# Optimization experiments

Hardware: AMD Instinct MI355X
Metric: run time of the kernel (lower is better)

## Reference

```python
import jax, jax.numpy as jnp
import numpy as np

B, S, DIM = 2, 2048, 2048
NH, NKV = 16, 8
HD = DIM // NH  # 128
ROPE_THETA = 10000.0


def setup_inputs() -> dict:
    key = jax.random.key(0)
    ks = jax.random.split(key, 7)
    std = DIM ** -0.5
    x = jax.random.normal(ks[0], (B, S, DIM), jnp.float32)
    wq = jax.random.normal(ks[1], (NH * HD, DIM), jnp.float32) * std
    wk = jax.random.normal(ks[2], (NKV * HD, DIM), jnp.float32) * std
    wv = jax.random.normal(ks[3], (NKV * HD, DIM), jnp.float32) * std
    wo = jax.random.normal(ks[4], (DIM, NH * HD), jnp.float32) * std
    inv_freq = 1.0 / (ROPE_THETA ** (jnp.arange(0, HD, 2, dtype=jnp.float32) / HD))
    ang = jnp.arange(S, dtype=jnp.float32)[:, None] * inv_freq[None, :]  # [S, HD//2]
    freqs_cos = jnp.cos(ang)
    freqs_sin = jnp.sin(ang)
    # diffusion-style random per-batch token mask: t ~ U[0,1) per batch row
    t = jax.random.uniform(ks[5], (B, 1))
    mask = jax.random.uniform(ks[6], (B, S)) < t  # True = masked key
    mask = mask.at[:, 0].set(False)  # first token never masked
    return dict(x=x, wq=wq, wk=wk, wv=wv, wo=wo,
                freqs_cos=freqs_cos, freqs_sin=freqs_sin, mask=mask)


def _rope(x, cos, sin):
    # x: [b, s, h, d]; pairs (x[2i], x[2i+1]) rotated by angle[s, i]
    xr, xi = x[..., 0::2], x[..., 1::2]
    c = cos[None, :, None, :]
    s = sin[None, :, None, :]
    out = jnp.stack([xr * c - xi * s, xr * s + xi * c], axis=-1)
    return out.reshape(x.shape)


def reference(x, wq, wk, wv, wo, freqs_cos, freqs_sin, mask):
    b, s, _ = x.shape
    xq = jnp.einsum('bsd,ed->bse', x, wq).reshape(b, s, NH, HD)
    xk = jnp.einsum('bsd,ed->bse', x, wk).reshape(b, s, NKV, HD)
    xv = jnp.einsum('bsd,ed->bse', x, wv).reshape(b, s, NKV, HD)
    xq = _rope(xq, freqs_cos, freqs_sin)
    xk = _rope(xk, freqs_cos, freqs_sin)
    n_rep = NH // NKV
    xk = jnp.repeat(xk, n_rep, axis=2)  # repeat_kv (GQA)
    xv = jnp.repeat(xv, n_rep, axis=2)
    q = xq.transpose(0, 2, 1, 3)  # [b, h, s, d]
    k = xk.transpose(0, 2, 1, 3)
    v = xv.transpose(0, 2, 1, 3)
    scale = 1.0 / np.sqrt(HD).astype(np.float32)
    scores = jnp.einsum('bhqd,bhkd->bhqk', q, k) * scale  # [b, h, s, s]
    scores = jnp.where(mask[:, None, None, :], -jnp.inf, scores)
    probs = jax.nn.softmax(scores, axis=-1)
    out = jnp.einsum('bhqk,bhkd->bhqd', probs, v)
    out = out.transpose(0, 2, 1, 3).reshape(b, s, NH * HD)
    return jnp.einsum('bse,de->bsd', out, wo)
```

## Files before the change

### kernel.cpp

```cpp
#include <hip/hip_runtime.h>
#include <hip/hip_bf16.h>
#include <cstdint>
#include <cstddef>

#define S_LEN   2048
#define NHQ     16
#define NKV_H   8
#define HD_DIM  128
#define DMODEL  2048
#define BATCH   2
#define KVD     (NKV_H * HD_DIM)
#define QKV_LD  4096

typedef float f32x4  __attribute__((ext_vector_type(4)));
typedef __bf16 bf16x8 __attribute__((ext_vector_type(8)));
typedef __bf16 bf16x4 __attribute__((ext_vector_type(4)));

__device__ __forceinline__ void gload_lds16(const __bf16* g, __bf16* l) {
    __builtin_amdgcn_global_load_lds(
        (const __attribute__((address_space(1))) void*)g,
        (__attribute__((address_space(3))) void*)l, 16, 0, 0);
}

__global__ void sniff_x_kernel(const unsigned* __restrict__ x,
                               int* __restrict__ flag) {
    __shared__ int cnt;
    if (threadIdx.x == 0) cnt = 0;
    __syncthreads();
    int c = 0;
    for (int j = threadIdx.x; j < 1024; j += 256) {
        unsigned hw = x[j] & 0xFFFFu;
        unsigned e  = (hw >> 7) & 0xFF;
        if (hw == 0u || (e >= 118 && e <= 132)) c++;
    }
    atomicAdd(&cnt, c);
    __syncthreads();
    if (threadIdx.x == 0) *flag = (cnt > 512) ? 1 : 0;
}

__global__ void sniff_fc_kernel(const unsigned* __restrict__ fc,
                                int* __restrict__ flag) {
    if (threadIdx.x == 0) *flag = (fc[0] == 0x3F803F80u) ? 1 : 0;
}

__global__ void mask_norm_kernel(const unsigned char* __restrict__ mraw,
                                 unsigned char* __restrict__ mout, int n) {
    __shared__ int f_bf16, f_f32, f_u8;
    if (threadIdx.x == 0) { f_bf16 = 0; f_f32 = 0; f_u8 = 0; }
    __syncthreads();
    const unsigned* dw = (const unsigned*)mraw;
    int ndw = n / 4;
    for (int j = threadIdx.x; j < ndw; j += blockDim.x) {
        unsigned v = dw[j];
        if (v == 0x00003F80u || v == 0x3F803F80u) f_bf16 = 1;
        else if (v == 0x3F800000u) f_f32 = 1;
        else if (v & 0xFFFFFFFEu) f_u8 = 1;
    }
    __syncthreads();
    int layout;
    if (f_bf16) layout = 3;
    else if (f_f32) layout = 2;
    else if (f_u8) layout = 0;
    else layout = 1;
    for (int i = threadIdx.x; i < n; i += blockDim.x) {
        unsigned v;
        if (layout == 0)      v = mraw[i];
        else if (layout == 3) v = ((const unsigned short*)mraw)[i];
        else                  v = ((const unsigned*)mraw)[i];
        mout[i] = v ? 1u : 0u;
    }
}

__global__ __launch_bounds__(256)
void conv_bf16_kernel(const void* __restrict__ src, __bf16* __restrict__ dst,
                      int n8, const int* __restrict__ dflag) {
    int i = blockIdx.x * blockDim.x + threadIdx.x;
    if (i >= n8) return;
    size_t off = (size_t)i * 8;
    if (*dflag) {
        *reinterpret_cast<uint4*>(dst + off) =
            *reinterpret_cast<const uint4*>((const __bf16*)src + off);
    } else {
        const float* f = (const float*)src + off;
        float4 a = *reinterpret_cast<const float4*>(f);
        float4 b = *reinterpret_cast<const float4*>(f + 4);
        bf16x8 v;
        v[0] = (__bf16)a.x; v[1] = (__bf16)a.y; v[2] = (__bf16)a.z; v[3] = (__bf16)a.w;
        v[4] = (__bf16)b.x; v[5] = (__bf16)b.y; v[6] = (__bf16)b.z; v[7] = (__bf16)b.w;
        *reinterpret_cast<bf16x8*>(dst + off) = v;
    }
}

__global__ __launch_bounds__(256)
void conv_bf16_strided_kernel(const void* __restrict__ src,
                              __bf16* __restrict__ dstbase,
                              int n8, const int* __restrict__ dflag) {
    int i = blockIdx.x * blockDim.x + threadIdx.x;
    if (i >= n8) return;
    size_t off = (size_t)i * 8;
    size_t row = off >> 11;
    size_t col = off & 2047;
    __bf16* dst = dstbase + row * QKV_LD + col;
    if (*dflag) {
        *reinterpret_cast<uint4*>(dst) =
            *reinterpret_cast<const uint4*>((const __bf16*)src + off);
    } else {
        const float* f = (const float*)src + off;
        float4 a = *reinterpret_cast<const float4*>(f);
        float4 b = *reinterpret_cast<const float4*>(f + 4);
        bf16x8 v;
        v[0] = (__bf16)a.x; v[1] = (__bf16)a.y; v[2] = (__bf16)a.z; v[3] = (__bf16)a.w;
        v[4] = (__bf16)b.x; v[5] = (__bf16)b.y; v[6] = (__bf16)b.z; v[7] = (__bf16)b.w;
        *reinterpret_cast<bf16x8*>(dst) = v;
    }
}

template <bool OUT_BF16>
__global__ __launch_bounds__(256)
void gemm_bt_async(const __bf16* __restrict__ A, const __bf16* __restrict__ Bw,
                   void* __restrict__ Cv, int K, int lda, int ldb, int ldc) {
    __shared__ __align__(16) __bf16 As[128 * 64];
    __shared__ __align__(16) __bf16 Bs[128 * 64];

    const int t    = threadIdx.x;
    const int w    = t >> 6;
    const int lane = t & 63;
    const int quad = lane >> 4;
    const int l16  = lane & 15;
    const int wm   = (w >> 1) * 64;
    const int wn   = (w & 1) * 64;
    const int m0   = blockIdx.x * 128;
    const int n0   = blockIdx.y * 128;
    const int rl   = lane >> 3;
    const int gl   = lane & 7;

    f32x4 acc[4][4];
#pragma unroll
    for (int i = 0; i < 4; ++i)
#pragma unroll
        for (int j = 0; j < 4; ++j) acc[i][j] = (f32x4){0.f, 0.f, 0.f, 0.f};

    for (int k0 = 0; k0 < K; k0 += 64) {
        __syncthreads();
#pragma unroll
        for (int p = 0; p < 4; ++p) {
            const int rowb = w * 32 + p * 8;
            const int r    = rowb + rl;
            const int gA   = gl ^ rl;
            gload_lds16(A  + (size_t)(m0 + r) * lda + k0 + gA * 8, &As[rowb * 64]);
            gload_lds16(Bw + (size_t)(n0 + r) * ldb + k0 + gA * 8, &Bs[rowb * 64]);
        }
        __syncthreads();
#pragma unroll
        for (int ks = 0; ks < 2; ++ks) {
            const int G = ks * 4 + quad;
            const int gsw = (G ^ (l16 & 7)) * 8;
            bf16x8 af[4], bf[4];
#pragma unroll
            for (int i = 0; i < 4; ++i)
                af[i] = *reinterpret_cast<const bf16x8*>(
                    &As[(wm + i * 16 + l16) * 64 + gsw]);
#pragma unroll
            for (int j = 0; j < 4; ++j)
                bf[j] = *reinterpret_cast<const bf16x8*>(
                    &Bs[(wn + j * 16 + l16) * 64 + gsw]);
#pragma unroll
            for (int i = 0; i < 4; ++i)
#pragma unroll
                for (int j = 0; j < 4; ++j)
                    acc[i][j] = __builtin_amdgcn_mfma_f32_16x16x32_bf16(
                        af[i], bf[j], acc[i][j], 0, 0, 0);
        }
    }
#pragma unroll
    for (int i = 0; i < 4; ++i)
#pragma unroll
        for (int r = 0; r < 4; ++r) {
            size_t m = (size_t)(m0 + wm + i * 16 + quad * 4 + r);
#pragma unroll
            for (int j = 0; j < 4; ++j) {
                int n = n0 + wn + j * 16 + l16;
                if constexpr (OUT_BF16)
                    ((__hip_bfloat16*)Cv)[m * ldc + n] = __float2bfloat16(acc[i][j][r]);
                else
                    ((float*)Cv)[m * ldc + n] = acc[i][j][r];
            }
        }
}

__global__ void rope_kernel(__hip_bfloat16* __restrict__ xqk,
                            const void* __restrict__ cosv,
                            const void* __restrict__ sinv,
                            const int* __restrict__ dflag_fc,
                            int npairs) {
    int idx = blockIdx.x * blockDim.x + threadIdx.x;
    if (idx >= npairs) return;
    int i  = idx & 63;
    int h  = (idx >> 6) % 24;
    int bs = idx / (64 * 24);
    int s  = bs & (S_LEN - 1);
    float c, sn;
    if (*dflag_fc) {
        c  = __bfloat162float(((const __hip_bfloat16*)cosv)[s * 64 + i]);
        sn = __bfloat162float(((const __hip_bfloat16*)sinv)[s * 64 + i]);
    } else {
        c  = ((const float*)cosv)[s * 64 + i];
        sn = ((const float*)sinv)[s * 64 + i];
    }
    unsigned* p = (unsigned*)(xqk + (size_t)bs * QKV_LD + h * HD_DIM) + i;
    unsigned u = *p;
    float xr = __uint_as_float(u << 16);
    float xi = __uint_as_float(u & 0xFFFF0000u);
    float o0 = xr * c - xi * sn;
    float o1 = xr * sn + xi * c;
    union { __hip_bfloat16 h2[2]; unsigned u32; } out;
    out.h2[0] = __float2bfloat16(o0);
    out.h2[1] = __float2bfloat16(o1);
    *p = out.u32;
}

__global__ __launch_bounds__(256)
void transpose_v_kernel(const __hip_bfloat16* __restrict__ xv,
                        __hip_bfloat16* __restrict__ vt) {
    __shared__ unsigned short T[32][36];
    const int t  = threadIdx.x;
    const int s0 = blockIdx.x * 32;
    const int d0 = blockIdx.y * 32;
    const int z  = blockIdx.z;
    const int b  = z >> 3;
    const int kv = z & 7;
    {
        int sr = t >> 3, dc = (t & 7) * 4;
        const unsigned short* p = (const unsigned short*)xv
            + (size_t)(b * S_LEN + s0 + sr) * QKV_LD + kv * 128 + d0 + dc;
        uint2 v = *reinterpret_cast<const uint2*>(p);
        T[sr][dc + 0] = (unsigned short)(v.x & 0xFFFFu);
        T[sr][dc + 1] = (unsigned short)(v.x >> 16);
        T[sr][dc + 2] = (unsigned short)(v.y & 0xFFFFu);
        T[sr][dc + 3] = (unsigned short)(v.y >> 16);
    }
    __syncthreads();
    {
        int dr = t >> 3, sc = (t & 7) * 4;
        unsigned w0 = (unsigned)T[sc + 0][dr] | ((unsigned)T[sc + 1][dr] << 16);
        unsigned w1 = (unsigned)T[sc + 2][dr] | ((unsigned)T[sc + 3][dr] << 16);
        unsigned short* q = (unsigned short*)vt
            + ((size_t)z * 128 + d0 + dr) * S_LEN + s0 + sc;
        uint2 v; v.x = w0; v.y = w1;
        *reinterpret_cast<uint2*>(q) = v;
    }
}

__global__ __launch_bounds__(256)
void attn_mfma2_kernel(__hip_bfloat16* qkv,
                       const __hip_bfloat16* __restrict__ vt_g,
                       const unsigned char* __restrict__ msk) {
    __shared__ __align__(16) __bf16 Ks[64 * 128];
    __shared__ __align__(16) __bf16 Vt[128 * 64];
    __shared__ __align__(16) __bf16 Ps[4][16][64];

    const int t    = threadIdx.x;
    const int w    = t >> 6;
    const int lane = t & 63;
    const int quad = lane >> 4;
    const int l16  = lane & 15;

    const int bid = blockIdx.x;
    const int qt  = bid & 31;
    const int h   = (bid >> 5) & (NHQ - 1);
    const int b   = bid >> 9;
    const int kvh = h >> 1;
    const int q0  = qt * 64;

    bf16x8 qf[4];
    {
        const __bf16* qrow = (const __bf16*)qkv
            + (size_t)(b * S_LEN + q0 + w * 16 + l16) * QKV_LD + h * 128 + quad * 8;
#pragma unroll
        for (int ks = 0; ks < 4; ++ks)
            qf[ks] = *reinterpret_cast<const bf16x8*>(qrow + ks * 32);
    }

    float m_r = -INFINITY, l_r = 0.f;
    f32x4 o[8];
#pragma unroll
    for (int d0 = 0; d0 < 8; ++d0) o[d0] = (f32x4){0.f, 0.f, 0.f, 0.f};

    const float scale2 = 0.08838834764831845f * 1.4426950408889634f;

    const __bf16* xk = (const __bf16*)qkv + 2048;

    const int krl = lane >> 4, kgl = lane & 15;
    const int vrl = lane >> 3, vgl = lane & 7;
    const int gbase = lane & 48;

    for (int k0 = 0; k0 < S_LEN; k0 += 64) {
        __syncthreads();
#pragma unroll
        for (int p = 0; p < 4; ++p) {
            const int row  = w * 16 + p * 4 + krl;
            const int srcg = kgl ^ (row & 7);
            gload_lds16(xk + (size_t)(b * S_LEN + k0 + row) * QKV_LD
                            + kvh * 128 + srcg * 8,
                        &Ks[(w * 16 + p * 4) * 128]);
        }
#pragma unroll
        for (int p = 0; p < 4; ++p) {
            const int row  = w * 32 + p * 8 + vrl;
            const int srcg = vgl ^ (row & 7);
            gload_lds16((const __bf16*)vt_g
                            + ((size_t)(b * NKV_H + kvh) * 128 + row) * S_LEN
                            + k0 + srcg * 8,
                        &Vt[(w * 32 + p * 8) * 64]);
        }
        unsigned mk4[4];
        {
            const unsigned* mp = (const unsigned*)(msk + b * S_LEN + k0);
#pragma unroll
            for (int n0 = 0; n0 < 4; ++n0) mk4[n0] = mp[n0 * 4 + quad];
        }
        __syncthreads();

        f32x4 sc4[4];
#pragma unroll
        for (int n0 = 0; n0 < 4; ++n0) sc4[n0] = (f32x4){0.f, 0.f, 0.f, 0.f};
        __builtin_amdgcn_s_setprio(1);
#pragma unroll
        for (int ks = 0; ks < 4; ++ks) {
            const int G = ks * 4 + quad;
#pragma unroll
            for (int n0 = 0; n0 < 4; ++n0) {
                const int row  = n0 * 16 + l16;
                const int slot = G ^ (row & 7);
                bf16x8 kf = *reinterpret_cast<const bf16x8*>(&Ks[row * 128 + slot * 8]);
                sc4[n0] = __builtin_amdgcn_mfma_f32_16x16x32_bf16(kf, qf[ks], sc4[n0], 0, 0, 0);
            }
        }
        __builtin_amdgcn_s_setprio(0);

#pragma unroll
        for (int n0 = 0; n0 < 4; ++n0)
#pragma unroll
            for (int r = 0; r < 4; ++r)
                sc4[n0][r] = ((mk4[n0] >> (r * 8)) & 0xFF) ? -INFINITY : sc4[n0][r];

        float tq[4];
#pragma unroll
        for (int n0 = 0; n0 < 4; ++n0)
            tq[n0] = fmaxf(fmaxf(sc4[n0][0], sc4[n0][1]),
                           fmaxf(sc4[n0][2], sc4[n0][3]));
        float rm = fmaxf(fmaxf(tq[0], tq[1]), fmaxf(tq[2], tq[3]));
        rm = fmaxf(rm, __shfl_xor(rm, 16, 64));
        rm = fmaxf(rm, __shfl_xor(rm, 32, 64));

        bool need = (rm - m_r) * scale2 > 8.0f;
        if (__any((int)need)) {
            float mn = fmaxf(m_r, rm);
            float al = exp2f((m_r - mn) * scale2);
            m_r = mn;
            l_r *= al;
            float alq[4];
#pragma unroll
            for (int r = 0; r < 4; ++r)
                alq[r] = __shfl(al, gbase | (quad * 4 + r), 64);
#pragma unroll
            for (int d0 = 0; d0 < 8; ++d0)
#pragma unroll
                for (int r = 0; r < 4; ++r) o[d0][r] *= alq[r];
        }

        float negm = -m_r * scale2;
#pragma unroll
        for (int n0 = 0; n0 < 4; ++n0)
#pragma unroll
            for (int r = 0; r < 4; ++r) {
                float p = exp2f(fmaf(sc4[n0][r], scale2, negm));
                sc4[n0][r] = p;
                l_r += p;
            }

#pragma unroll
        for (int n0 = 0; n0 < 4; ++n0) {
            const int kb    = n0 * 16 + quad * 4;
            const int gran  = kb >> 3;
            const int half4 = kb & 4;
            const int slot  = gran ^ (l16 & 7);
            bf16x4 pk;
            pk[0] = (__bf16)sc4[n0][0];
            pk[1] = (__bf16)sc4[n0][1];
            pk[2] = (__bf16)sc4[n0][2];
            pk[3] = (__bf16)sc4[n0][3];
            *reinterpret_cast<bf16x4*>(&Ps[w][l16][slot * 8 + half4]) = pk;
        }

        __builtin_amdgcn_s_setprio(1);
#pragma unroll
        for (int kk = 0; kk < 64; kk += 32) {
            const int Gp    = (kk >> 3) + quad;
            const int slotp = Gp ^ (l16 & 7);
            bf16x8 af = *reinterpret_cast<const bf16x8*>(&Ps[w][l16][slotp * 8]);
#pragma unroll
            for (int d0 = 0; d0 < 8; ++d0) {
                const int row  = d0 * 16 + l16;
                const int slot = Gp ^ (row & 7);
                bf16x8 bf = *reinterpret_cast<const bf16x8*>(&Vt[row * 64 + slot * 8]);
                o[d0] = __builtin_amdgcn_mfma_f32_16x16x32_bf16(af, bf, o[d0], 0, 0, 0);
            }
        }
        __builtin_amdgcn_s_setprio(0);
    }

    float ls = l_r;
    ls += __shfl_xor(ls, 16, 64);
    ls += __shfl_xor(ls, 32, 64);
    float invl = 1.f / ls;
    float invq[4];
#pragma unroll
    for (int r = 0; r < 4; ++r)
        invq[r] = __shfl(invl, gbase | (quad * 4 + r), 64);
    __hip_bfloat16* att = qkv;
#pragma unroll
    for (int d0 = 0; d0 < 8; ++d0)
#pragma unroll
        for (int r = 0; r < 4; ++r) {
            size_t row = (size_t)(b * S_LEN + q0 + w * 16 + quad * 4 + r);
            att[row * QKV_LD + h * 128 + d0 * 16 + l16] =
                __float2bfloat16(o[d0][r] * invq[r]);
        }
}

extern "C" void kernel_launch(void* const* d_in, const int* in_sizes, int n_in,
                              void* d_out, int out_size, void* d_ws, size_t ws_size,
                              hipStream_t stream) {
    const void* x  = d_in[0];
    const void* wq = d_in[1];
    const void* wk = d_in[2];
    const void* wv = d_in[3];
    const void* wo = d_in[4];
    const void* fc = d_in[5];
    const void* fs = d_in[6];
    const unsigned char* mraw = (const unsigned char*)d_in[7];

    const int M = BATCH * S_LEN;
    char* wsb = (char*)d_ws;
    int* dflag_x  = (int*)wsb;
    int* dflag_fc = (int*)(wsb + 64);
    unsigned char* mnorm = (unsigned char*)(wsb + 128);
    __hip_bfloat16* qkv = (__hip_bfloat16*)(wsb + 8192);

    char* dob = (char*)d_out;
    __bf16* xb    = (__bf16*)dob;
    __bf16* wcomb = (__bf16*)(dob + (16u << 20));
    __bf16* wqb = wcomb;
    __bf16* wkb = wcomb + (size_t)2048 * 2048;
    __bf16* wvb = wcomb + (size_t)3072 * 2048;
    __hip_bfloat16* vt = (__hip_bfloat16*)d_out;

    hipLaunchKernelGGL(sniff_x_kernel, dim3(1), dim3(256), 0, stream,
                       (const unsigned*)x, dflag_x);
    hipLaunchKernelGGL(sniff_fc_kernel, dim3(1), dim3(64), 0, stream,
                       (const unsigned*)fc, dflag_fc);
    hipLaunchKernelGGL(mask_norm_kernel, dim3(1), dim3(256), 0, stream,
                       mraw, mnorm, BATCH * S_LEN);

    hipLaunchKernelGGL(conv_bf16_kernel, dim3((M * DMODEL / 8) / 256), dim3(256), 0, stream,
                       x, xb, M * DMODEL / 8, dflag_x);
    hipLaunchKernelGGL(conv_bf16_kernel, dim3((DMODEL * DMODEL / 8) / 256), dim3(256), 0, stream,
                       wq, wqb, DMODEL * DMODEL / 8, dflag_x);
    hipLaunchKernelGGL(conv_bf16_kernel, dim3((KVD * DMODEL / 8) / 256), dim3(256), 0, stream,
                       wk, wkb, KVD * DMODEL / 8, dflag_x);
    hipLaunchKernelGGL(conv_bf16_kernel, dim3((KVD * DMODEL / 8) / 256), dim3(256), 0, stream,
                       wv, wvb, KVD * DMODEL / 8, dflag_x);

    hipLaunchKernelGGL((gemm_bt_async<true>), dim3(M / 128, QKV_LD / 128), dim3(256), 0, stream,
                       xb, wcomb, (void*)qkv, DMODEL, DMODEL, DMODEL, QKV_LD);

    int npairs = M * 24 * (HD_DIM / 2);
    hipLaunchKernelGGL(rope_kernel, dim3(npairs / 256), dim3(256), 0, stream,
                       qkv, fc, fs, dflag_fc, npairs);

    hipLaunchKernelGGL(transpose_v_kernel, dim3(S_LEN / 32, HD_DIM / 32, BATCH * NKV_H),
                       dim3(256), 0, stream, qkv + 3072, vt);

    hipLaunchKernelGGL(attn_mfma2_kernel, dim3(BATCH * NHQ * (S_LEN / 64)), dim3(256), 0, stream,
                       qkv, vt, mnorm);

    hipLaunchKernelGGL(conv_bf16_strided_kernel, dim3((DMODEL * DMODEL / 8) / 256), dim3(256), 0, stream,
                       wo, (__bf16*)qkv + 2048, DMODEL * DMODEL / 8, dflag_x);

    hipLaunchKernelGGL((gemm_bt_async<false>), dim3(M / 128, DMODEL / 128), dim3(256), 0, stream,
                       (const __bf16*)qkv, (const __bf16*)qkv + 2048, d_out,
                       DMODEL, QKV_LD, QKV_LD, DMODEL);
}
```

Measured before the change: 434.6 us.

## Double attention query tile per block and swizzle block order for cache locality

Each attention block now handles 128 query rows, with every wave processing two 16-row groups, so each loaded K/V tile and K fragment read from LDS feeds twice as many MFMAs. The grid halves to 512 blocks, and block IDs are permuted so neighbouring blocks share a head and its KV data across XCDs. The GEMM also gets an XCD-aware block index swizzle to improve L2 reuse. The cost is higher register pressure from doubled accumulators and fewer blocks to fill the device.

```diff
diff --git a/kernel.cpp b/kernel.cpp
--- a/kernel.cpp
+++ b/kernel.cpp
@@ -129,8 +129,13 @@
     const int l16  = lane & 15;
     const int wm   = (w >> 1) * 64;
     const int wn   = (w & 1) * 64;
-    const int m0   = blockIdx.x * 128;
-    const int n0   = blockIdx.y * 128;
+
+    const int nwg  = gridDim.x * gridDim.y;
+    const int lin  = blockIdx.y * gridDim.x + blockIdx.x;
+    const int swz  = (lin & 7) * (nwg >> 3) + (lin >> 3);
+    const int m0   = (swz % gridDim.x) * 128;
+    const int n0   = (swz / gridDim.x) * 128;
+
     const int rl   = lane >> 3;
     const int gl   = lane & 7;
 
@@ -257,7 +262,7 @@
                        const unsigned char* __restrict__ msk) {
     __shared__ __align__(16) __bf16 Ks[64 * 128];
     __shared__ __align__(16) __bf16 Vt[128 * 64];
-    __shared__ __align__(16) __bf16 Ps[4][16][64];
+    __shared__ __align__(16) __bf16 Ps[4][32][64];
 
     const int t    = threadIdx.x;
     const int w    = t >> 6;
@@ -265,65 +270,83 @@
     const int quad = lane >> 4;
     const int l16  = lane & 15;
 
-    const int bid = blockIdx.x;
-    const int qt  = bid & 31;
-    const int h   = (bid >> 5) & (NHQ - 1);
-    const int b   = bid >> 9;
+    const int bid = ((blockIdx.x & 7) << 6) | (blockIdx.x >> 3);
+    const int qt  = bid & 15;
+    const int h   = (bid >> 4) & (NHQ - 1);
+    const int b   = bid >> 8;
     const int kvh = h >> 1;
-    const int q0  = qt * 64;
-
-    bf16x8 qf[4];
+    const int q0  = qt * 128;
+
+    bf16x8 qf[2][4];
     {
         const __bf16* qrow = (const __bf16*)qkv
-            + (size_t)(b * S_LEN + q0 + w * 16 + l16) * QKV_LD + h * 128 + quad * 8;
-#pragma unroll
-        for (int ks = 0; ks < 4; ++ks)
-            qf[ks] = *reinterpret_cast<const bf16x8*>(qrow + ks * 32);
-    }
-
-    float m_r = -INFINITY, l_r = 0.f;
-    f32x4 o[8];
-#pragma unroll
-    for (int d0 = 0; d0 < 8; ++d0) o[d0] = (f32x4){0.f, 0.f, 0.f, 0.f};
+            + (size_t)(b * S_LEN + q0 + w * 32 + l16) * QKV_LD + h * 128 + quad * 8;
+#pragma unroll
+        for (int g = 0; g < 2; ++g)
+#pragma unroll
+            for (int ks = 0; ks < 4; ++ks)
+                qf[g][ks] = *reinterpret_cast<const bf16x8*>(
+                    qrow + (size_t)g * 16 * QKV_LD + ks * 32);
+    }
+
+    float m_r[2], l_r[2];
+    f32x4 o[2][8];
+#pragma unroll
+    for (int g = 0; g < 2; ++g) {
+        m_r[g] = -INFINITY; l_r[g] = 0.f;
+#pragma unroll
+        for (int d0 = 0; d0 < 8; ++d0) o[g][d0] = (f32x4){0.f, 0.f, 0.f, 0.f};
+    }
 
     const float scale2 = 0.08838834764831845f * 1.4426950408889634f;
-
-    const __bf16* xk = (const __bf16*)qkv + 2048;
-
-    const int krl = lane >> 4, kgl = lane & 15;
-    const int vrl = lane >> 3, vgl = lane & 7;
     const int gbase = lane & 48;
+
+    const __bf16* kp[4];
+    const __bf16* vp[4];
+    {
+        const __bf16* xk = (const __bf16*)qkv + 2048;
+        const int krl = lane >> 4, kgl = lane & 15;
+        const int vrl = lane >> 3, vgl = lane & 7;
+#pragma unroll
+        for (int p = 0; p < 4; ++p) {
+            const int row = w * 16 + p * 4 + krl;
+            kp[p] = xk + (size_t)(b * S_LEN + row) * QKV_LD
+                       + kvh * 128 + (kgl ^ (row & 7)) * 8;
+        }
+#pragma unroll
+        for (int p = 0; p < 4; ++p) {
+            const int row = w * 32 + p * 8 + vrl;
+            vp[p] = (const __bf16*)vt_g
+                  + ((size_t)(b * NKV_H + kvh) * 128 + row) * S_LEN
+                  + (vgl ^ (row & 7)) * 8;
+        }
+    }
+    const unsigned char* mbase = msk + b * S_LEN;
 
     for (int k0 = 0; k0 < S_LEN; k0 += 64) {
         __syncthreads();
 #pragma unroll
-        for (int p = 0; p < 4; ++p) {
-            const int row  = w * 16 + p * 4 + krl;
-            const int srcg = kgl ^ (row & 7);
-            gload_lds16(xk + (size_t)(b * S_LEN + k0 + row) * QKV_LD
-                            + kvh * 128 + srcg * 8,
-                        &Ks[(w * 16 + p * 4) * 128]);
-        }
-#pragma unroll
-        for (int p = 0; p < 4; ++p) {
-            const int row  = w * 32 + p * 8 + vrl;
-            const int srcg = vgl ^ (row & 7);
-            gload_lds16((const __bf16*)vt_g
-                            + ((size_t)(b * NKV_H + kvh) * 128 + row) * S_LEN
-                            + k0 + srcg * 8,
-                        &Vt[(w * 32 + p * 8) * 64]);
-        }
+        for (int p = 0; p < 4; ++p)
+            gload_lds16(kp[p], &Ks[(w * 16 + p * 4) * 128]);
+#pragma unroll
+        for (int p = 0; p < 4; ++p)
+            gload_lds16(vp[p], &Vt[(w * 32 + p * 8) * 64]);
+#pragma unroll
+        for (int p = 0; p < 4; ++p) { kp[p] += 64 * QKV_LD; vp[p] += 64; }
+
         unsigned mk4[4];
         {
-            const unsigned* mp = (const unsigned*)(msk + b * S_LEN + k0);
+            const unsigned* mp = (const unsigned*)(mbase + k0);
 #pragma unroll
             for (int n0 = 0; n0 < 4; ++n0) mk4[n0] = mp[n0 * 4 + quad];
         }
         __syncthreads();
 
-        f32x4 sc4[4];
-#pragma unroll
-        for (int n0 = 0; n0 < 4; ++n0) sc4[n0] = (f32x4){0.f, 0.f, 0.f, 0.f};
+        f32x4 sc[2][4];
+#pragma unroll
+        for (int g = 0; g < 2; ++g)
+#pragma unroll
+            for (int n0 = 0; n0 < 4; ++n0) sc[g][n0] = (f32x4){0.f, 0.f, 0.f, 0.f};
         __builtin_amdgcn_s_setprio(1);
 #pragma unroll
         for (int ks = 0; ks < 4; ++ks) {
@@ -333,64 +356,72 @@
                 const int row  = n0 * 16 + l16;
                 const int slot = G ^ (row & 7);
                 bf16x8 kf = *reinterpret_cast<const bf16x8*>(&Ks[row * 128 + slot * 8]);
-                sc4[n0] = __builtin_amdgcn_mfma_f32_16x16x32_bf16(kf, qf[ks], sc4[n0], 0, 0, 0);
+                sc[0][n0] = __builtin_amdgcn_mfma_f32_16x16x32_bf16(kf, qf[0][ks], sc[0][n0], 0, 0, 0);
+                sc[1][n0] = __builtin_amdgcn_mfma_f32_16x16x32_bf16(kf, qf[1][ks], sc[1][n0], 0, 0, 0);
             }
         }
         __builtin_amdgcn_s_setprio(0);
 
-#pragma unroll
-        for (int n0 = 0; n0 < 4; ++n0)
-#pragma unroll
-            for (int r = 0; r < 4; ++r)
-                sc4[n0][r] = ((mk4[n0] >> (r * 8)) & 0xFF) ? -INFINITY : sc4[n0][r];
-
-        float tq[4];
-#pragma unroll
-        for (int n0 = 0; n0 < 4; ++n0)
-            tq[n0] = fmaxf(fmaxf(sc4[n0][0], sc4[n0][1]),
-                           fmaxf(sc4[n0][2], sc4[n0][3]));
-        float rm = fmaxf(fmaxf(tq[0], tq[1]), fmaxf(tq[2], tq[3]));
-        rm = fmaxf(rm, __shfl_xor(rm, 16, 64));
-        rm = fmaxf(rm, __shfl_xor(rm, 32, 64));
-
-        bool need = (rm - m_r) * scale2 > 8.0f;
+        float rm[2];
+#pragma unroll
+        for (int g = 0; g < 2; ++g) {
+#pragma unroll
+            for (int n0 = 0; n0 < 4; ++n0)
+#pragma unroll
+                for (int r = 0; r < 4; ++r)
+                    sc[g][n0][r] = ((mk4[n0] >> (r * 8)) & 0xFF) ? -INFINITY : sc[g][n0][r];
+            float tq0 = fmaxf(fmaxf(sc[g][0][0], sc[g][0][1]), fmaxf(sc[g][0][2], sc[g][0][3]));
+            float tq1 = fmaxf(fmaxf(sc[g][1][0], sc[g][1][1]), fmaxf(sc[g][1][2], sc[g][1][3]));
+            float tq2 = fmaxf(fmaxf(sc[g][2][0], sc[g][2][1]), fmaxf(sc[g][2][2], sc[g][2][3]));
+            float tq3 = fmaxf(fmaxf(sc[g][3][0], sc[g][3][1]), fmaxf(sc[g][3][2], sc[g][3][3]));
+            float m4 = fmaxf(fmaxf(tq0, tq1), fmaxf(tq2, tq3));
+            m4 = fmaxf(m4, __shfl_xor(m4, 16, 64));
+            m4 = fmaxf(m4, __shfl_xor(m4, 32, 64));
+            rm[g] = m4;
+        }
+
+        bool need = ((rm[0] - m_r[0]) * scale2 > 8.0f) ||
+                    ((rm[1] - m_r[1]) * scale2 > 8.0f);
         if (__any((int)need)) {
-            float mn = fmaxf(m_r, rm);
-            float al = exp2f((m_r - mn) * scale2);
-            m_r = mn;
-            l_r *= al;
-            float alq[4];
-#pragma unroll
-            for (int r = 0; r < 4; ++r)
-                alq[r] = __shfl(al, gbase | (quad * 4 + r), 64);
-#pragma unroll
-            for (int d0 = 0; d0 < 8; ++d0)
-#pragma unroll
-                for (int r = 0; r < 4; ++r) o[d0][r] *= alq[r];
-        }
-
-        float negm = -m_r * scale2;
-#pragma unroll
-        for (int n0 = 0; n0 < 4; ++n0)
-#pragma unroll
-            for (int r = 0; r < 4; ++r) {
-                float p = exp2f(fmaf(sc4[n0][r], scale2, negm));
-                sc4[n0][r] = p;
-                l_r += p;
+#pragma unroll
+            for (int g = 0; g < 2; ++g) {
+                float mn = fmaxf(m_r[g], rm[g]);
+                float al = exp2f((m_r[g] - mn) * scale2);
+                m_r[g] = mn;
+                l_r[g] *= al;
+                float alq[4];
+#pragma unroll
+                for (int r = 0; r < 4; ++r)
+                    alq[r] = __shfl(al, gbase | (quad * 4 + r), 64);
+#pragma unroll
+                for (int d0 = 0; d0 < 8; ++d0)
+#pragma unroll
+                    for (int r = 0; r < 4; ++r) o[g][d0][r] *= alq[r];
             }
-
-#pragma unroll
-        for (int n0 = 0; n0 < 4; ++n0) {
-            const int kb    = n0 * 16 + quad * 4;
-            const int gran  = kb >> 3;
-            const int half4 = kb & 4;
-            const int slot  = gran ^ (l16 & 7);
-            bf16x4 pk;
-            pk[0] = (__bf16)sc4[n0][0];
-            pk[1] = (__bf16)sc4[n0][1];
-            pk[2] = (__bf16)sc4[n0][2];
-            pk[3] = (__bf16)sc4[n0][3];
-            *reinterpret_cast<bf16x4*>(&Ps[w][l16][slot * 8 + half4]) = pk;
+        }
+
+#pragma unroll
+        for (int g = 0; g < 2; ++g) {
+            float negm = -m_r[g] * scale2;
+#pragma unroll
+            for (int n0 = 0; n0 < 4; ++n0) {
+#pragma unroll
+                for (int r = 0; r < 4; ++r) {
+                    float p = exp2f(fmaf(sc[g][n0][r], scale2, negm));
+                    sc[g][n0][r] = p;
+                    l_r[g] += p;
+                }
+                const int kb    = n0 * 16 + quad * 4;
+                const int gran  = kb >> 3;
+                const int half4 = kb & 4;
+                const int slot  = gran ^ (l16 & 7);
+                bf16x4 pk;
+                pk[0] = (__bf16)sc[g][n0][0];
+                pk[1] = (__bf16)sc[g][n0][1];
+                pk[2] = (__bf16)sc[g][n0][2];
+                pk[3] = (__bf16)sc[g][n0][3];
+                *reinterpret_cast<bf16x4*>(&Ps[w][g * 16 + l16][slot * 8 + half4]) = pk;
+            }
         }
 
         __builtin_amdgcn_s_setprio(1);
@@ -398,35 +429,40 @@
         for (int kk = 0; kk < 64; kk += 32) {
             const int Gp    = (kk >> 3) + quad;
             const int slotp = Gp ^ (l16 & 7);
-            bf16x8 af = *reinterpret_cast<const bf16x8*>(&Ps[w][l16][slotp * 8]);
+            bf16x8 af0 = *reinterpret_cast<const bf16x8*>(&Ps[w][l16][slotp * 8]);
+            bf16x8 af1 = *reinterpret_cast<const bf16x8*>(&Ps[w][16 + l16][slotp * 8]);
 #pragma unroll
             for (int d0 = 0; d0 < 8; ++d0) {
                 const int row  = d0 * 16 + l16;
                 const int slot = Gp ^ (row & 7);
                 bf16x8 bf = *reinterpret_cast<const bf16x8*>(&Vt[row * 64 + slot * 8]);
-                o[d0] = __builtin_amdgcn_mfma_f32_16x16x32_bf16(af, bf, o[d0], 0, 0, 0);
+                o[0][d0] = __builtin_amdgcn_mfma_f32_16x16x32_bf16(af0, bf, o[0][d0], 0, 0, 0);
+                o[1][d0] = __builtin_amdgcn_mfma_f32_16x16x32_bf16(af1, bf, o[1][d0], 0, 0, 0);
             }
         }
         __builtin_amdgcn_s_setprio(0);
     }
 
-    float ls = l_r;
-    ls += __shfl_xor(ls, 16, 64);
-    ls += __shfl_xor(ls, 32, 64);
-    float invl = 1.f / ls;
-    float invq[4];
-#pragma unroll
-    for (int r = 0; r < 4; ++r)
-        invq[r] = __shfl(invl, gbase | (quad * 4 + r), 64);
     __hip_bfloat16* att = qkv;
 #pragma unroll
-    for (int d0 = 0; d0 < 8; ++d0)
-#pragma unroll
-        for (int r = 0; r < 4; ++r) {
-            size_t row = (size_t)(b * S_LEN + q0 + w * 16 + quad * 4 + r);
-            att[row * QKV_LD + h * 128 + d0 * 16 + l16] =
-                __float2bfloat16(o[d0][r] * invq[r]);
-        }
+    for (int g = 0; g < 2; ++g) {
+        float ls = l_r[g];
+        ls += __shfl_xor(ls, 16, 64);
+        ls += __shfl_xor(ls, 32, 64);
+        float invl = 1.f / ls;
+        float invq[4];
+#pragma unroll
+        for (int r = 0; r < 4; ++r)
+            invq[r] = __shfl(invl, gbase | (quad * 4 + r), 64);
+#pragma unroll
+        for (int d0 = 0; d0 < 8; ++d0)
+#pragma unroll
+            for (int r = 0; r < 4; ++r) {
+                size_t row = (size_t)(b * S_LEN + q0 + w * 32 + g * 16 + quad * 4 + r);
+                att[row * QKV_LD + h * 128 + d0 * 16 + l16] =
+                    __float2bfloat16(o[g][d0][r] * invq[r]);
+            }
+    }
 }
 
 extern "C" void kernel_launch(void* const* d_in, const int* in_sizes, int n_in,
@@ -482,7 +518,7 @@
     hipLaunchKernelGGL(transpose_v_kernel, dim3(S_LEN / 32, HD_DIM / 32, BATCH * NKV_H),
                        dim3(256), 0, stream, qkv + 3072, vt);
 
-    hipLaunchKernelGGL(attn_mfma2_kernel, dim3(BATCH * NHQ * (S_LEN / 64)), dim3(256), 0, stream,
+    hipLaunchKernelGGL(attn_mfma2_kernel, dim3(BATCH * NHQ * (S_LEN / 128)), dim3(256), 0, stream,
                        qkv, vt, mnorm);
 
     hipLaunchKernelGGL(conv_bf16_strided_kernel, dim3((DMODEL * DMODEL / 8) / 256), dim3(256), 0, stream,
```

After: 468.5 us. +7.8%, slower.
